# Optimization experiments

Hardware: AMD Instinct MI355X
Metric: run time of the kernel (lower is better)

Reference implementation:

```python
import jax, jax.numpy as jnp
import numpy as np

B, TQ, TK = 32, 2000, 512
BLANK_LOGPROB = -1.0
NEG = -1e9  # stand-in for -inf, safe under logsumexp grads


def setup_inputs() -> dict:
    key = jax.random.key(0)
    k1, k2, k3 = jax.random.split(key, 3)
    attn_logprob = jax.random.normal(k1, (B, TQ, TK), dtype=jnp.float32)
    in_lens = jax.random.randint(k2, (B,), 1, TK + 1, dtype=jnp.int32)
    # query (mel) lengths >= key (text) lengths so the CTC alignment exists
    out_lens = jax.random.randint(k3, (B,), TK, TQ + 1, dtype=jnp.int32)
    return {"attn_logprob": attn_logprob, "in_lens": in_lens, "out_lens": out_lens}


def _forward_sum_loss(attn_logprob, in_lens, out_lens):
    # attn_logprob: [B, Tq, Tk]
    Bb, Tq, Tk = attn_logprob.shape
    kl = jnp.clip(in_lens, 1, Tk).astype(jnp.int32)      # target lengths
    ql = jnp.clip(out_lens, 1, Tq).astype(jnp.int32)     # input lengths

    # pad a blank column at key index 0 (blank logit = blank_logprob)
    padded = jnp.pad(attn_logprob, ((0, 0), (0, 0), (1, 0)),
                     constant_values=BLANK_LOGPROB)       # [B, Tq, Tk+1]
    # per-sample log_softmax over the first kl+1 key entries (masked softmax)
    key_mask = jnp.arange(Tk + 1)[None, :] <= kl[:, None]  # [B, Tk+1]
    logp = jax.nn.log_softmax(jnp.where(key_mask[:, None, :], padded, NEG), axis=-1)

    # CTC with targets = [1..kl] (all distinct), blank = 0.
    # Extended state sequence: blank,1,blank,2,...,blank,kl,blank -> 2*kl+1 states.
    S = 2 * Tk + 1
    s = jnp.arange(S)
    label_idx = jnp.where(s % 2 == 1, (s + 1) // 2, 0)          # emission index per state
    state_valid = s[None, :] < (2 * kl[:, None] + 1)            # [B, S]
    skip_ok = (s % 2 == 1) & (s >= 2)                           # distinct labels -> skip allowed

    e0 = logp[:, 0, label_idx]                                  # [B, S]
    alpha0 = jnp.full((Bb, S), NEG, dtype=logp.dtype)
    alpha0 = alpha0.at[:, 0].set(e0[:, 0]).at[:, 1].set(e0[:, 1])

    def step(alpha, xs):
        logp_t, t = xs                                          # logp_t: [B, Tk+1]
        e_t = logp_t[:, label_idx]                              # [B, S]
        p0 = alpha
        p1 = jnp.pad(alpha[:, :-1], ((0, 0), (1, 0)), constant_values=NEG)
        p2 = jnp.pad(alpha[:, :-2], ((0, 0), (2, 0)), constant_values=NEG)
        p2 = jnp.where(skip_ok[None, :], p2, NEG)
        new = jax.nn.logsumexp(jnp.stack([p0, p1, p2]), axis=0) + e_t
        new = jnp.where(state_valid, new, NEG)
        alpha = jnp.where((t < ql)[:, None], new, alpha)        # freeze past each ql
        return alpha, None

    xs = (jnp.moveaxis(logp[:, 1:, :], 0, 1), jnp.arange(1, Tq))
    alpha, _ = jax.lax.scan(step, alpha0, xs)

    end = 2 * kl                                                # final blank state
    a_end = jnp.take_along_axis(alpha, end[:, None], axis=1)[:, 0]
    a_lab = jnp.take_along_axis(alpha, (end - 1)[:, None], axis=1)[:, 0]
    ll = jnp.logaddexp(a_end, a_lab)
    # torch CTCLoss(reduction='mean') with batch 1 divides by target length
    loss = -ll / kl.astype(attn_logprob.dtype)
    return jnp.mean(loss)


def reference(attn_logprob, in_lens, out_lens):
    return _forward_sum_loss(attn_logprob, in_lens, out_lens)
```

## Files before the change

### kernel.cpp

```cpp
#include <hip/hip_runtime.h>
#include <math.h>

#define BB 32
#define TQQ 2000
#define TKK 512
#define CR 8
#define RS 8
#define NW 8
#define SLOT_F 520
#define BRN 32

__device__ __forceinline__ float dpp_mv_111(float x, float old) {
    return __int_as_float(__builtin_amdgcn_update_dpp(__float_as_int(old), __float_as_int(x), 0x111, 0xf, 0xf, false));
}
__device__ __forceinline__ float dpp_mv_112(float x, float old) {
    return __int_as_float(__builtin_amdgcn_update_dpp(__float_as_int(old), __float_as_int(x), 0x112, 0xf, 0xf, false));
}
__device__ __forceinline__ float dpp_mv_114(float x, float old) {
    return __int_as_float(__builtin_amdgcn_update_dpp(__float_as_int(old), __float_as_int(x), 0x114, 0xf, 0xf, false));
}
__device__ __forceinline__ float dpp_mv_118(float x, float old) {
    return __int_as_float(__builtin_amdgcn_update_dpp(__float_as_int(old), __float_as_int(x), 0x118, 0xf, 0xf, false));
}
__device__ __forceinline__ float dpp_mv_b15(float x, float old) {
    return __int_as_float(__builtin_amdgcn_update_dpp(__float_as_int(old), __float_as_int(x), 0x142, 0xf, 0xf, false));
}
__device__ __forceinline__ float dpp_mv_b31(float x, float old) {
    return __int_as_float(__builtin_amdgcn_update_dpp(__float_as_int(old), __float_as_int(x), 0x143, 0xf, 0xf, false));
}
__device__ __forceinline__ float dpp_wave_shr1(float x, float old) {
    return __int_as_float(__builtin_amdgcn_update_dpp(__float_as_int(old), __float_as_int(x), 0x138, 0xf, 0xf, false));
}

__device__ __forceinline__ float wred_max(float x) {
    x = fmaxf(x, dpp_mv_111(x, -1e38f));
    x = fmaxf(x, dpp_mv_112(x, -1e38f));
    x = fmaxf(x, dpp_mv_114(x, -1e38f));
    x = fmaxf(x, dpp_mv_118(x, -1e38f));
    x = fmaxf(x, dpp_mv_b15(x, -1e38f));
    x = fmaxf(x, dpp_mv_b31(x, -1e38f));
    return __int_as_float(__builtin_amdgcn_readlane(__float_as_int(x), 63));
}
__device__ __forceinline__ float wred_sum(float x) {
    x += dpp_mv_111(x, 0.0f);
    x += dpp_mv_112(x, 0.0f);
    x += dpp_mv_114(x, 0.0f);
    x += dpp_mv_118(x, 0.0f);
    x += dpp_mv_b15(x, 0.0f);
    x += dpp_mv_b31(x, 0.0f);
    return __int_as_float(__builtin_amdgcn_readlane(__float_as_int(x), 63));
}

__device__ __forceinline__ float pow2i(int e) {
    return __int_as_float((unsigned)(e + 127) << 23);
}

__device__ __forceinline__ void step_quad(float4 p, float pb, float o_prev,
                                          float E[4], float O[4]) {
    float t3 = E[3] + O[2];  O[3] = (O[3] + t3) * p.w;  E[3] = t3 * pb;
    float t2 = E[2] + O[1];  O[2] = (O[2] + t2) * p.z;  E[2] = t2 * pb;
    float t1 = E[1] + O[0];  O[1] = (O[1] + t1) * p.y;  E[1] = t1 * pb;
    float t0 = E[0] + o_prev; O[0] = (O[0] + t0) * p.x; E[0] = t0 * pb;
}

__global__ __launch_bounds__(NW * 64)
void ForwardSumLoss_77378130805413_kernel(const float* __restrict__ attn,
                                          const int* __restrict__ in_lens,
                                          const int* __restrict__ out_lens,
                                          float* __restrict__ out)
{
    __shared__ float s_slots[RS * CR * SLOT_F];
    __shared__ float s_dumpE[513];
    __shared__ float s_dumpO[512];
    __shared__ float s_bring[BRN];
    __shared__ int   s_ef0[4];
    __shared__ int   s_ready[RS];
    __shared__ int   s_w0, s_w1;
    __shared__ int   s_e0c, s_e1c;

    const int b    = blockIdx.x;
    const int tid  = threadIdx.x;
    const int wave = tid >> 6;
    const int lane = tid & 63;

    int kl = in_lens[b];  kl = kl < 1 ? 1 : (kl > TKK ? TKK : kl);
    int ql = out_lens[b]; ql = ql < 1 ? 1 : (ql > TQQ ? TQQ : ql);
    const int nchunks = (ql + CR - 1) / CR;

    if (tid < RS)  s_ready[tid] = -1;
    if (tid < BRN) s_bring[tid] = 0.f;
    if (tid == 32) s_w0 = -1;
    if (tid == 33) s_w1 = -1;
    __syncthreads();

    volatile int* vready = s_ready;
    volatile int* vw0    = &s_w0;
    volatile int* vw1    = &s_w1;
    volatile int* vEF0   = s_ef0;

    const float T = 1.0995116e12f;

    if (wave == 0) {
        __builtin_amdgcn_s_setprio(3);
        float E[4] = {0,0,0,0}, O[4] = {0,0,0,0};
        int e0c = 0;
        const int base4 = 4 * lane;
        int rdyN = -9, w1s = -9;

        for (int k = 0; k < nchunks; ++k) {
            const int t0   = k * CR;
            const int rows = min(ql - t0, CR);
            if (k >= 2) { while (w1s < k - 2) { w1s = *vw1; } }
            if (rdyN != k) { while (vready[k & (RS - 1)] != k) {} }
            asm volatile("" ::: "memory");
            const float* bp = s_slots + (size_t)(k & (RS - 1)) * CR * SLOT_F;

            if (rows == CR) {
                float4 P[CR]; float PB[CR];
                #pragma unroll
                for (int r = 0; r < CR; ++r) {
                    P[r]  = *(const float4*)(bp + r * SLOT_F + base4);
                    PB[r] = bp[r * SLOT_F + 512];
                }
                rdyN = vready[(k + 1) & (RS - 1)];
                w1s  = *vw1;
                #pragma unroll
                for (int r = 0; r < CR; ++r) {
                    if (k == 0 && r == 0) {
                        E[0] = (lane == 0) ? PB[0]  * T : 0.f;
                        O[0] = (lane == 0) ? P[0].x * T : 0.f;
                    } else {
                        float o_prev = dpp_wave_shr1(O[3], 0.0f);
                        step_quad(P[r], PB[r], o_prev, E, O);
                    }
                    if (r < CR - 1) { if (lane == 63) s_bring[(t0 + r) & (BRN - 1)] = O[3]; }
                }
                float m0 = fmaxf(fmaxf(fmaxf(E[0], E[1]), fmaxf(E[2], E[3])),
                                 fmaxf(fmaxf(O[0], O[1]), fmaxf(O[2], O[3])));
                m0 = wred_max(m0);
                int ef = 0;
                if (m0 > 0.f) ef = 167 - (int)((__float_as_uint(m0) >> 23) & 255);
                float fh = pow2i(ef - (ef >> 1));
                float fl = pow2i(ef >> 1);
                #pragma unroll
                for (int i = 0; i < 4; ++i) { E[i] = (E[i] * fh) * fl; O[i] = (O[i] * fh) * fl; }
                e0c += ef;
                if (lane == 0) vEF0[k & 3] = ef;
                if (lane == 63) s_bring[(t0 + CR - 1) & (BRN - 1)] = O[3];
            } else {
                for (int r = 0; r < rows; ++r) {
                    const float* sq = bp + r * SLOT_F;
                    float4 p = *(const float4*)(sq + base4);
                    float pb = sq[512];
                    if (k == 0 && r == 0) {
                        E[0] = (lane == 0) ? pb  * T : 0.f;
                        O[0] = (lane == 0) ? p.x * T : 0.f;
                    } else {
                        float o_prev = dpp_wave_shr1(O[3], 0.0f);
                        step_quad(p, pb, o_prev, E, O);
                    }
                    if (lane == 63) s_bring[(t0 + r) & (BRN - 1)] = O[3];
                }
            }
            asm volatile("" ::: "memory");
            if (lane == 0) *vw0 = k;
        }
        #pragma unroll
        for (int i = 0; i < 4; ++i) {
            s_dumpE[base4 + i] = E[i];
            s_dumpO[base4 + i] = O[i];
        }
        if (lane == 0) s_e0c = e0c;
    } else if (wave == 1) {
        __builtin_amdgcn_s_setprio(3);
        float E[4] = {0,0,0,0}, O[4] = {0,0,0,0}, e512 = 0.f;
        int e0c = 0, e1c = 0;
        const int base4 = 256 + 4 * lane;
        int w0s = -9;

        for (int k = 0; k < nchunks; ++k) {
            const int t0   = k * CR;
            const int rows = min(ql - t0, CR);
            while (w0s < k) { w0s = *vw0; }
            asm volatile("" ::: "memory");
            const float* bp = s_slots + (size_t)(k & (RS - 1)) * CR * SLOT_F;

            int dE = e1c - e0c;
            dE = dE < -250 ? -250 : (dE > 250 ? 250 : dE);
            const float Ch = pow2i(dE - (dE >> 1));
            const float Cl = pow2i(dE >> 1);

            if (rows == CR) {
                float4 P[CR]; float PB[CR], BND[CR];
                #pragma unroll
                for (int r = 0; r < CR; ++r) {
                    P[r]   = *(const float4*)(bp + r * SLOT_F + base4);
                    PB[r]  = bp[r * SLOT_F + 512];
                    BND[r] = (s_bring[(t0 - 1 + r) & (BRN - 1)] * Ch) * Cl;
                }
                w0s = *vw0;
                #pragma unroll
                for (int r = 0; r < CR; ++r) {
                    float o_prev = dpp_wave_shr1(O[3], 0.0f);
                    o_prev = (lane == 0) ? BND[r] : o_prev;
                    float te = e512 + O[3]; e512 = te * PB[r];
                    step_quad(P[r], PB[r], o_prev, E, O);
                }
                float m1 = fmaxf(fmaxf(fmaxf(E[0], E[1]), fmaxf(E[2], E[3])),
                                 fmaxf(fmaxf(O[0], O[1]), fmaxf(O[2], O[3])));
                m1 = fmaxf(m1, e512);
                m1 = wred_max(m1);
                int ef0k = vEF0[k & 3];
                int ef1  = (m1 > 0.f) ? (167 - (int)((__float_as_uint(m1) >> 23) & 255))
                                      : ef0k;
                float fh = pow2i(ef1 - (ef1 >> 1));
                float fl = pow2i(ef1 >> 1);
                #pragma unroll
                for (int i = 0; i < 4; ++i) { E[i] = (E[i] * fh) * fl; O[i] = (O[i] * fh) * fl; }
                e512 = (e512 * fh) * fl;
                e1c += ef1;
                e0c += ef0k;
            } else {
                for (int r = 0; r < rows; ++r) {
                    const float* sq = bp + r * SLOT_F;
                    float4 p = *(const float4*)(sq + base4);
                    float pb = sq[512];
                    float bnd = (s_bring[(t0 - 1 + r) & (BRN - 1)] * Ch) * Cl;
                    float o_prev = dpp_wave_shr1(O[3], 0.0f);
                    o_prev = (lane == 0) ? bnd : o_prev;
                    float te = e512 + O[3]; e512 = te * pb;
                    step_quad(p, pb, o_prev, E, O);
                }
            }
            asm volatile("" ::: "memory");
            if (lane == 0) *vw1 = k;
        }
        #pragma unroll
        for (int i = 0; i < 4; ++i) {
            s_dumpE[base4 + i] = E[i];
            s_dumpO[base4 + i] = O[i];
        }
        if (lane == 63) s_dumpE[512] = e512;
        if (lane == 0)  s_e1c = e1c;
    } else {
        const int pidx = wave - 2;
        const float* base = attn + (size_t)b * TQQ * TKK;
        const int j0 = 8 * lane;

        for (int c = pidx; c < nchunks; c += NW - 2) {
            const int t0 = c * CR;
            while (*vw1 < c - RS) { __builtin_amdgcn_s_sleep(4); }
            asm volatile("" ::: "memory");

            float4 x0[CR], x1[CR];
            #pragma unroll
            for (int r = 0; r < CR; ++r) {
                x0[r] = make_float4(-1e30f, -1e30f, -1e30f, -1e30f);
                x1[r] = x0[r];
                const int t = t0 + r;
                if (t < ql) {
                    const float* row = base + (size_t)t * TKK;
                    if (j0 < kl)     x0[r] = *(const float4*)(row + j0);
                    if (j0 + 4 < kl) x1[r] = *(const float4*)(row + j0 + 4);
                }
            }
            float* bp = s_slots + (size_t)(c & (RS - 1)) * CR * SLOT_F;
            #pragma unroll
            for (int r = 0; r < CR; ++r) {
                const int t = t0 + r;
                if (t >= ql) continue;
                float va[8] = {x0[r].x, x0[r].y, x0[r].z, x0[r].w,
                               x1[r].x, x1[r].y, x1[r].z, x1[r].w};
                float m = -1.0f;
                #pragma unroll
                for (int cc = 0; cc < 8; ++cc) if (j0 + cc < kl) m = fmaxf(m, va[cc]);
                m = wred_max(m);
                float pv[8]; float vsum = 0.f;
                #pragma unroll
                for (int cc = 0; cc < 8; ++cc) {
                    pv[cc] = (j0 + cc < kl) ? __expf(va[cc] - m) : 0.f;
                    vsum += pv[cc];
                }
                vsum = wred_sum(vsum);
                float vb   = __expf(-1.0f - m);
                float rinv = 1.0f / (vsum + vb);
                float* sp = bp + (size_t)r * SLOT_F;
                *(float4*)(sp + j0)     = make_float4(pv[0]*rinv, pv[1]*rinv, pv[2]*rinv, pv[3]*rinv);
                *(float4*)(sp + j0 + 4) = make_float4(pv[4]*rinv, pv[5]*rinv, pv[6]*rinv, pv[7]*rinv);
                if (lane == 0) sp[512] = vb * rinv;
            }
            __threadfence_block();
            if (lane == 0) vready[c & (RS - 1)] = c;
        }
    }

    __syncthreads();
    if (tid == 0) {
        const double logTd = 27.725887222397812;
        const double LN2d  = 0.69314718055994531;
        float aE = s_dumpE[kl];
        float aO = s_dumpO[kl - 1];
        int e0c = s_e0c, e1c = s_e1c;
        double sE = logTd + (double)((kl     >= 256) ? e1c : e0c) * LN2d;
        double sO = logTd + (double)((kl - 1 >= 256) ? e1c : e0c) * LN2d;
        double lE = (aE > 0.f) ? log((double)aE) - sE : -1e300;
        double lO = (aO > 0.f) ? log((double)aO) - sO : -1e300;
        double mx = fmax(lE, lO);
        double ll = (mx < -1e290) ? -745.0 : mx + log(exp(lE - mx) + exp(lO - mx));
        float val = (float)(-ll / ((double)kl * (double)BB));
        atomicAdd(out, val);
    }
}

extern "C" void kernel_launch(void* const* d_in, const int* in_sizes, int n_in,
                              void* d_out, int out_size, void* d_ws, size_t ws_size,
                              hipStream_t stream) {
    const float* attn     = (const float*)d_in[0];
    const int*   in_lens  = (const int*)d_in[1];
    const int*   out_lens = (const int*)d_in[2];
    float* out = (float*)d_out;
    hipMemsetAsync(out, 0, sizeof(float), stream);
    hipLaunchKernelGGL(ForwardSumLoss_77378130805413_kernel,
                       dim3(BB), dim3(NW * 64), 0, stream,
                       attn, in_lens, out_lens, out);
}
```

Measured before the change: 370.5 us.

## Double-buffer LDS reads in recurrence waves with inline asm prefetch of next chunk

Both recurrence waves now prefetch the next chunk's probabilities, blank probs, boundary values and exponent offsets into a second register set with inline ds_read_b128, then wait on lgkmcnt before computing. This hides LDS latency behind the serial DP step. Blank probabilities and boundary carries move to contiguous per-slot arrays so each can be fetched as two vector reads. The producer/consumer lead between waves is relaxed from 2 to LEAD=5 chunks. In exchange, register pressure rises and correctness now depends on hand-managed waitcnt and sched_barrier ordering.

```diff
diff --git a/kernel.cpp b/kernel.cpp
--- a/kernel.cpp
+++ b/kernel.cpp
@@ -8,7 +8,11 @@
 #define RS 8
 #define NW 8
 #define SLOT_F 520
-#define BRN 32
+#define LEAD 5
+
+typedef float f32x4 __attribute__((ext_vector_type(4)));
+
+#define AS3F(p) ((const __attribute__((address_space(3))) float*)(p))
 
 __device__ __forceinline__ float dpp_mv_111(float x, float old) {
     return __int_as_float(__builtin_amdgcn_update_dpp(__float_as_int(old), __float_as_int(x), 0x111, 0xf, 0xf, false));
@@ -55,7 +59,7 @@
     return __int_as_float((unsigned)(e + 127) << 23);
 }
 
-__device__ __forceinline__ void step_quad(float4 p, float pb, float o_prev,
+__device__ __forceinline__ void step_quad(f32x4 p, float pb, float o_prev,
                                           float E[4], float O[4]) {
     float t3 = E[3] + O[2];  O[3] = (O[3] + t3) * p.w;  E[3] = t3 * pb;
     float t2 = E[2] + O[1];  O[2] = (O[2] + t2) * p.z;  E[2] = t2 * pb;
@@ -70,10 +74,11 @@
                                           float* __restrict__ out)
 {
     __shared__ float s_slots[RS * CR * SLOT_F];
+    __shared__ float s_pb[RS * CR];
+    __shared__ float s_bringS[RS * CR];
     __shared__ float s_dumpE[513];
     __shared__ float s_dumpO[512];
-    __shared__ float s_bring[BRN];
-    __shared__ int   s_ef0[4];
+    __shared__ int   s_ef0[RS];
     __shared__ int   s_ready[RS];
     __shared__ int   s_w0, s_w1;
     __shared__ int   s_e0c, s_e1c;
@@ -85,12 +90,13 @@
 
     int kl = in_lens[b];  kl = kl < 1 ? 1 : (kl > TKK ? TKK : kl);
     int ql = out_lens[b]; ql = ql < 1 ? 1 : (ql > TQQ ? TQQ : ql);
+    const int fullc   = ql >> 3;
     const int nchunks = (ql + CR - 1) / CR;
 
     if (tid < RS)  s_ready[tid] = -1;
-    if (tid < BRN) s_bring[tid] = 0.f;
-    if (tid == 32) s_w0 = -1;
-    if (tid == 33) s_w1 = -1;
+    if (tid >= 64 && tid < 64 + RS * CR) s_bringS[tid - 64] = 0.f;
+    if (tid == 128) s_w0 = -1;
+    if (tid == 129) s_w1 = -1;
     __syncthreads();
 
     volatile int* vready = s_ready;
@@ -105,66 +111,113 @@
         float E[4] = {0,0,0,0}, O[4] = {0,0,0,0};
         int e0c = 0;
         const int base4 = 4 * lane;
-        int rdyN = -9, w1s = -9;
-
-        for (int k = 0; k < nchunks; ++k) {
-            const int t0   = k * CR;
-            const int rows = min(ql - t0, CR);
-            if (k >= 2) { while (w1s < k - 2) { w1s = *vw1; } }
-            if (rdyN != k) { while (vready[k & (RS - 1)] != k) {} }
-            asm volatile("" ::: "memory");
-            const float* bp = s_slots + (size_t)(k & (RS - 1)) * CR * SLOT_F;
-
-            if (rows == CR) {
-                float4 P[CR]; float PB[CR];
-                #pragma unroll
-                for (int r = 0; r < CR; ++r) {
-                    P[r]  = *(const float4*)(bp + r * SLOT_F + base4);
-                    PB[r] = bp[r * SLOT_F + 512];
+        const unsigned aSlot0 = (unsigned)(unsigned long long)AS3F(s_slots) + (unsigned)(base4 * 4);
+        const unsigned aPbB   = (unsigned)(unsigned long long)AS3F(s_pb);
+        int rdyN = -9, w1s = -1;
+        int k = 0;
+
+        f32x4 A0={0,0,0,0},A1={0,0,0,0},A2={0,0,0,0},A3={0,0,0,0},A4={0,0,0,0},A5={0,0,0,0},A6={0,0,0,0},A7={0,0,0,0},Ap0={0,0,0,0},Ap1={0,0,0,0};
+        f32x4 B0={0,0,0,0},B1={0,0,0,0},B2={0,0,0,0},B3={0,0,0,0},B4={0,0,0,0},B5={0,0,0,0},B6={0,0,0,0},B7={0,0,0,0},Bp0={0,0,0,0},Bp1={0,0,0,0};
+
+#define W0_ISSUE(S, kk) do {                                                  \
+    unsigned a_ = aSlot0 + (unsigned)((((kk) & (RS - 1)) * CR * SLOT_F) * 4); \
+    asm volatile("ds_read_b128 %0, %1 offset:0"     : "=v"(S##0) : "v"(a_));  \
+    asm volatile("ds_read_b128 %0, %1 offset:2080"  : "=v"(S##1) : "v"(a_));  \
+    asm volatile("ds_read_b128 %0, %1 offset:4160"  : "=v"(S##2) : "v"(a_));  \
+    asm volatile("ds_read_b128 %0, %1 offset:6240"  : "=v"(S##3) : "v"(a_));  \
+    asm volatile("ds_read_b128 %0, %1 offset:8320"  : "=v"(S##4) : "v"(a_));  \
+    asm volatile("ds_read_b128 %0, %1 offset:10400" : "=v"(S##5) : "v"(a_));  \
+    asm volatile("ds_read_b128 %0, %1 offset:12480" : "=v"(S##6) : "v"(a_));  \
+    asm volatile("ds_read_b128 %0, %1 offset:14560" : "=v"(S##7) : "v"(a_));  \
+    unsigned q_ = aPbB + (unsigned)((((kk) & (RS - 1)) * CR) * 4);            \
+    asm volatile("ds_read_b128 %0, %1 offset:0"  : "=v"(S##p0) : "v"(q_));    \
+    asm volatile("ds_read_b128 %0, %1 offset:16" : "=v"(S##p1) : "v"(q_));    \
+} while (0)
+
+#define W0_STEP(CUR, NXT)                                                     \
+    do {                                                                      \
+        asm volatile("s_waitcnt lgkmcnt(0)" ::: "memory");                    \
+        __builtin_amdgcn_sched_barrier(0);                                    \
+        if (k + 1 < fullc) {                                                  \
+            if (rdyN != k + 1) {                                              \
+                do { rdyN = vready[(k + 1) & (RS - 1)]; } while (rdyN != k + 1); \
+                asm volatile("" ::: "memory");                                \
+            }                                                                 \
+            W0_ISSUE(NXT, k + 1);                                             \
+            __builtin_amdgcn_sched_barrier(0);                                \
+        }                                                                     \
+        if (w1s < k - LEAD) {                                                 \
+            do { w1s = *vw1; } while (w1s < k - LEAD);                        \
+            asm volatile("" ::: "memory");                                    \
+        }                                                                     \
+        {                                                                     \
+            f32x4 PA_[CR] = {CUR##0, CUR##1, CUR##2, CUR##3,                  \
+                             CUR##4, CUR##5, CUR##6, CUR##7};                 \
+            float PB_[CR] = {CUR##p0.x, CUR##p0.y, CUR##p0.z, CUR##p0.w,      \
+                             CUR##p1.x, CUR##p1.y, CUR##p1.z, CUR##p1.w};     \
+            _Pragma("unroll")                                                 \
+            for (int r = 0; r < CR; ++r) {                                    \
+                if (k == 0 && r == 0) {                                       \
+                    E[0] = (lane == 0) ? PB_[0]   * T : 0.f;                  \
+                    O[0] = (lane == 0) ? PA_[0].x * T : 0.f;                  \
+                } else {                                                      \
+                    float o_prev = dpp_wave_shr1(O[3], 0.0f);                 \
+                    step_quad(PA_[r], PB_[r], o_prev, E, O);                  \
+                }                                                             \
+                if (r < CR - 1) { if (lane == 63) s_bringS[(k & (RS - 1)) * CR + r] = O[3]; } \
+            }                                                                 \
+            float m0_ = fmaxf(fmaxf(fmaxf(E[0], E[1]), fmaxf(E[2], E[3])),    \
+                              fmaxf(fmaxf(O[0], O[1]), fmaxf(O[2], O[3])));   \
+            m0_ = wred_max(m0_);                                              \
+            int ef_ = 0;                                                      \
+            if (m0_ > 0.f) ef_ = 167 - (int)((__float_as_uint(m0_) >> 23) & 255); \
+            float fh_ = pow2i(ef_ - (ef_ >> 1));                              \
+            float fl_ = pow2i(ef_ >> 1);                                      \
+            _Pragma("unroll")                                                 \
+            for (int i = 0; i < 4; ++i) { E[i] = (E[i]*fh_)*fl_; O[i] = (O[i]*fh_)*fl_; } \
+            e0c += ef_;                                                       \
+            if (lane == 0) vEF0[k & (RS - 1)] = ef_;                          \
+            if (lane == 63) s_bringS[(k & (RS - 1)) * CR + (CR - 1)] = O[3];  \
+        }                                                                     \
+        asm volatile("" ::: "memory");                                        \
+        if (lane == 0) *vw0 = k;                                              \
+        w1s  = *vw1;                                                          \
+        rdyN = vready[(k + 2) & (RS - 1)];                                    \
+    } while (0)
+
+        if (fullc > 0) {
+            while (vready[0] != 0) {}
+            asm volatile("" ::: "memory");
+            W0_ISSUE(A, 0);
+            for (;;) {
+                W0_STEP(A, B); if (++k >= fullc) break;
+                W0_STEP(B, A); if (++k >= fullc) break;
+            }
+        }
+        if (nchunks > fullc) {
+            const int rows = ql - k * CR;
+            if (w1s < k - LEAD) { do { w1s = *vw1; } while (w1s < k - LEAD); }
+            while (vready[k & (RS - 1)] != k) {}
+            asm volatile("" ::: "memory");
+            const float* bp  = s_slots + (size_t)(k & (RS - 1)) * CR * SLOT_F;
+            const float* pbb = s_pb + (k & (RS - 1)) * CR;
+            for (int r = 0; r < rows; ++r) {
+                f32x4 pl = *(const f32x4*)(bp + r * SLOT_F + base4);
+                float pb = pbb[r];
+                if (k == 0 && r == 0) {
+                    E[0] = (lane == 0) ? pb   * T : 0.f;
+                    O[0] = (lane == 0) ? pl.x * T : 0.f;
+                } else {
+                    float o_prev = dpp_wave_shr1(O[3], 0.0f);
+                    step_quad(pl, pb, o_prev, E, O);
                 }
-                rdyN = vready[(k + 1) & (RS - 1)];
-                w1s  = *vw1;
-                #pragma unroll
-                for (int r = 0; r < CR; ++r) {
-                    if (k == 0 && r == 0) {
-                        E[0] = (lane == 0) ? PB[0]  * T : 0.f;
-                        O[0] = (lane == 0) ? P[0].x * T : 0.f;
-                    } else {
-                        float o_prev = dpp_wave_shr1(O[3], 0.0f);
-                        step_quad(P[r], PB[r], o_prev, E, O);
-                    }
-                    if (r < CR - 1) { if (lane == 63) s_bring[(t0 + r) & (BRN - 1)] = O[3]; }
-                }
-                float m0 = fmaxf(fmaxf(fmaxf(E[0], E[1]), fmaxf(E[2], E[3])),
-                                 fmaxf(fmaxf(O[0], O[1]), fmaxf(O[2], O[3])));
-                m0 = wred_max(m0);
-                int ef = 0;
-                if (m0 > 0.f) ef = 167 - (int)((__float_as_uint(m0) >> 23) & 255);
-                float fh = pow2i(ef - (ef >> 1));
-                float fl = pow2i(ef >> 1);
-                #pragma unroll
-                for (int i = 0; i < 4; ++i) { E[i] = (E[i] * fh) * fl; O[i] = (O[i] * fh) * fl; }
-                e0c += ef;
-                if (lane == 0) vEF0[k & 3] = ef;
-                if (lane == 63) s_bring[(t0 + CR - 1) & (BRN - 1)] = O[3];
-            } else {
-                for (int r = 0; r < rows; ++r) {
-                    const float* sq = bp + r * SLOT_F;
-                    float4 p = *(const float4*)(sq + base4);
-                    float pb = sq[512];
-                    if (k == 0 && r == 0) {
-                        E[0] = (lane == 0) ? pb  * T : 0.f;
-                        O[0] = (lane == 0) ? p.x * T : 0.f;
-                    } else {
-                        float o_prev = dpp_wave_shr1(O[3], 0.0f);
-                        step_quad(p, pb, o_prev, E, O);
-                    }
-                    if (lane == 63) s_bring[(t0 + r) & (BRN - 1)] = O[3];
-                }
+                if (lane == 63) s_bringS[(k & (RS - 1)) * CR + r] = O[3];
             }
             asm volatile("" ::: "memory");
             if (lane == 0) *vw0 = k;
         }
+#undef W0_STEP
+#undef W0_ISSUE
         #pragma unroll
         for (int i = 0; i < 4; ++i) {
             s_dumpE[base4 + i] = E[i];
@@ -173,68 +226,126 @@
         if (lane == 0) s_e0c = e0c;
     } else if (wave == 1) {
         __builtin_amdgcn_s_setprio(3);
-        float E[4] = {0,0,0,0}, O[4] = {0,0,0,0}, e512 = 0.f;
+        float E[4] = {0,0,0,0}, O[4] = {0,0,0,0}, e512 = 0.f, prev7 = 0.f;
         int e0c = 0, e1c = 0;
         const int base4 = 256 + 4 * lane;
-        int w0s = -9;
-
-        for (int k = 0; k < nchunks; ++k) {
-            const int t0   = k * CR;
-            const int rows = min(ql - t0, CR);
+        const unsigned aSlot0 = (unsigned)(unsigned long long)AS3F(s_slots) + (unsigned)(base4 * 4);
+        const unsigned aPbB   = (unsigned)(unsigned long long)AS3F(s_pb);
+        const unsigned aBrB   = (unsigned)(unsigned long long)AS3F(s_bringS);
+        const unsigned aEfB   = (unsigned)(unsigned long long)AS3F((const float*)s_ef0);
+        int w0s = -1;
+        int k = 0;
+
+        f32x4 A0={0,0,0,0},A1={0,0,0,0},A2={0,0,0,0},A3={0,0,0,0},A4={0,0,0,0},A5={0,0,0,0},A6={0,0,0,0},A7={0,0,0,0},Ap0={0,0,0,0},Ap1={0,0,0,0},Ab0={0,0,0,0},Ab1={0,0,0,0};
+        f32x4 B0={0,0,0,0},B1={0,0,0,0},B2={0,0,0,0},B3={0,0,0,0},B4={0,0,0,0},B5={0,0,0,0},B6={0,0,0,0},B7={0,0,0,0},Bp0={0,0,0,0},Bp1={0,0,0,0},Bb0={0,0,0,0},Bb1={0,0,0,0};
+        int Ae_ = 0, Be_ = 0;
+
+#define W1_ISSUE(S, kk) do {                                                  \
+    unsigned a_ = aSlot0 + (unsigned)((((kk) & (RS - 1)) * CR * SLOT_F) * 4); \
+    asm volatile("ds_read_b128 %0, %1 offset:0"     : "=v"(S##0) : "v"(a_));  \
+    asm volatile("ds_read_b128 %0, %1 offset:2080"  : "=v"(S##1) : "v"(a_));  \
+    asm volatile("ds_read_b128 %0, %1 offset:4160"  : "=v"(S##2) : "v"(a_));  \
+    asm volatile("ds_read_b128 %0, %1 offset:6240"  : "=v"(S##3) : "v"(a_));  \
+    asm volatile("ds_read_b128 %0, %1 offset:8320"  : "=v"(S##4) : "v"(a_));  \
+    asm volatile("ds_read_b128 %0, %1 offset:10400" : "=v"(S##5) : "v"(a_));  \
+    asm volatile("ds_read_b128 %0, %1 offset:12480" : "=v"(S##6) : "v"(a_));  \
+    asm volatile("ds_read_b128 %0, %1 offset:14560" : "=v"(S##7) : "v"(a_));  \
+    unsigned q_ = aPbB + (unsigned)((((kk) & (RS - 1)) * CR) * 4);            \
+    asm volatile("ds_read_b128 %0, %1 offset:0"  : "=v"(S##p0) : "v"(q_));    \
+    asm volatile("ds_read_b128 %0, %1 offset:16" : "=v"(S##p1) : "v"(q_));    \
+    unsigned r_ = aBrB + (unsigned)((((kk) & (RS - 1)) * CR) * 4);            \
+    asm volatile("ds_read_b128 %0, %1 offset:0"  : "=v"(S##b0) : "v"(r_));    \
+    asm volatile("ds_read_b128 %0, %1 offset:16" : "=v"(S##b1) : "v"(r_));    \
+    unsigned e_ = aEfB + (unsigned)(((kk) & (RS - 1)) * 4);                   \
+    asm volatile("ds_read_b32 %0, %1" : "=v"(S##e_) : "v"(e_));               \
+} while (0)
+
+#define W1_STEP(CUR, NXT)                                                     \
+    do {                                                                      \
+        asm volatile("s_waitcnt lgkmcnt(0)" ::: "memory");                    \
+        __builtin_amdgcn_sched_barrier(0);                                    \
+        if (k + 1 < fullc) {                                                  \
+            if (w0s < k + 1) {                                                \
+                do { w0s = *vw0; } while (w0s < k + 1);                       \
+                asm volatile("" ::: "memory");                                \
+            }                                                                 \
+            W1_ISSUE(NXT, k + 1);                                             \
+            __builtin_amdgcn_sched_barrier(0);                                \
+        }                                                                     \
+        {                                                                     \
+            int dE_ = e1c - e0c;                                              \
+            dE_ = dE_ < -250 ? -250 : (dE_ > 250 ? 250 : dE_);                \
+            const float Ch_ = pow2i(dE_ - (dE_ >> 1));                        \
+            const float Cl_ = pow2i(dE_ >> 1);                                \
+            int ef0k_ = CUR##e_;                                              \
+            f32x4 PA_[CR] = {CUR##0, CUR##1, CUR##2, CUR##3,                  \
+                             CUR##4, CUR##5, CUR##6, CUR##7};                 \
+            float PB_[CR] = {CUR##p0.x, CUR##p0.y, CUR##p0.z, CUR##p0.w,      \
+                             CUR##p1.x, CUR##p1.y, CUR##p1.z, CUR##p1.w};     \
+            float BR_[CR] = {prev7, CUR##b0.x, CUR##b0.y, CUR##b0.z,          \
+                             CUR##b0.w, CUR##b1.x, CUR##b1.y, CUR##b1.z};     \
+            _Pragma("unroll")                                                 \
+            for (int r = 0; r < CR; ++r) {                                    \
+                float bnd_ = (BR_[r] * Ch_) * Cl_;                            \
+                float o_prev = dpp_wave_shr1(O[3], 0.0f);                     \
+                o_prev = (lane == 0) ? bnd_ : o_prev;                         \
+                float te_ = e512 + O[3]; e512 = te_ * PB_[r];                 \
+                step_quad(PA_[r], PB_[r], o_prev, E, O);                      \
+            }                                                                 \
+            float m1_ = fmaxf(fmaxf(fmaxf(E[0], E[1]), fmaxf(E[2], E[3])),    \
+                              fmaxf(fmaxf(O[0], O[1]), fmaxf(O[2], O[3])));   \
+            m1_ = fmaxf(m1_, e512);                                           \
+            m1_ = wred_max(m1_);                                              \
+            int ef1_ = (m1_ > 0.f) ? (167 - (int)((__float_as_uint(m1_) >> 23) & 255)) \
+                                   : ef0k_;                                   \
+            float fh_ = pow2i(ef1_ - (ef1_ >> 1));                            \
+            float fl_ = pow2i(ef1_ >> 1);                                     \
+            _Pragma("unroll")                                                 \
+            for (int i = 0; i < 4; ++i) { E[i] = (E[i]*fh_)*fl_; O[i] = (O[i]*fh_)*fl_; } \
+            e512 = (e512 * fh_) * fl_;                                        \
+            e1c += ef1_;                                                      \
+            e0c += ef0k_;                                                     \
+            prev7 = CUR##b1.w;                                                \
+        }                                                                     \
+        asm volatile("" ::: "memory");                                        \
+        if (lane == 0) *vw1 = k;                                              \
+        w0s = *vw0;                                                           \
+    } while (0)
+
+        if (fullc > 0) {
+            do { w0s = *vw0; } while (w0s < 0);
+            asm volatile("" ::: "memory");
+            W1_ISSUE(A, 0);
+            for (;;) {
+                W1_STEP(A, B); if (++k >= fullc) break;
+                W1_STEP(B, A); if (++k >= fullc) break;
+            }
+        }
+        if (nchunks > fullc) {
+            const int rows = ql - k * CR;
             while (w0s < k) { w0s = *vw0; }
             asm volatile("" ::: "memory");
-            const float* bp = s_slots + (size_t)(k & (RS - 1)) * CR * SLOT_F;
-
             int dE = e1c - e0c;
             dE = dE < -250 ? -250 : (dE > 250 ? 250 : dE);
             const float Ch = pow2i(dE - (dE >> 1));
             const float Cl = pow2i(dE >> 1);
-
-            if (rows == CR) {
-                float4 P[CR]; float PB[CR], BND[CR];
-                #pragma unroll
-                for (int r = 0; r < CR; ++r) {
-                    P[r]   = *(const float4*)(bp + r * SLOT_F + base4);
-                    PB[r]  = bp[r * SLOT_F + 512];
-                    BND[r] = (s_bring[(t0 - 1 + r) & (BRN - 1)] * Ch) * Cl;
-                }
-                w0s = *vw0;
-                #pragma unroll
-                for (int r = 0; r < CR; ++r) {
-                    float o_prev = dpp_wave_shr1(O[3], 0.0f);
-                    o_prev = (lane == 0) ? BND[r] : o_prev;
-                    float te = e512 + O[3]; e512 = te * PB[r];
-                    step_quad(P[r], PB[r], o_prev, E, O);
-                }
-                float m1 = fmaxf(fmaxf(fmaxf(E[0], E[1]), fmaxf(E[2], E[3])),
-                                 fmaxf(fmaxf(O[0], O[1]), fmaxf(O[2], O[3])));
-                m1 = fmaxf(m1, e512);
-                m1 = wred_max(m1);
-                int ef0k = vEF0[k & 3];
-                int ef1  = (m1 > 0.f) ? (167 - (int)((__float_as_uint(m1) >> 23) & 255))
-                                      : ef0k;
-                float fh = pow2i(ef1 - (ef1 >> 1));
-                float fl = pow2i(ef1 >> 1);
-                #pragma unroll
-                for (int i = 0; i < 4; ++i) { E[i] = (E[i] * fh) * fl; O[i] = (O[i] * fh) * fl; }
-                e512 = (e512 * fh) * fl;
-                e1c += ef1;
-                e0c += ef0k;
-            } else {
-                for (int r = 0; r < rows; ++r) {
-                    const float* sq = bp + r * SLOT_F;
-                    float4 p = *(const float4*)(sq + base4);
-                    float pb = sq[512];
-                    float bnd = (s_bring[(t0 - 1 + r) & (BRN - 1)] * Ch) * Cl;
-                    float o_prev = dpp_wave_shr1(O[3], 0.0f);
-                    o_prev = (lane == 0) ? bnd : o_prev;
-                    float te = e512 + O[3]; e512 = te * pb;
-                    step_quad(p, pb, o_prev, E, O);
-                }
+            const float* bp  = s_slots + (size_t)(k & (RS - 1)) * CR * SLOT_F;
+            const float* pbb = s_pb + (k & (RS - 1)) * CR;
+            for (int r = 0; r < rows; ++r) {
+                f32x4 pl = *(const f32x4*)(bp + r * SLOT_F + base4);
+                float pb = pbb[r];
+                float braw = (r == 0) ? prev7 : s_bringS[(k & (RS - 1)) * CR + (r - 1)];
+                float bnd = (braw * Ch) * Cl;
+                float o_prev = dpp_wave_shr1(O[3], 0.0f);
+                o_prev = (lane == 0) ? bnd : o_prev;
+                float te = e512 + O[3]; e512 = te * pb;
+                step_quad(pl, pb, o_prev, E, O);
             }
             asm volatile("" ::: "memory");
             if (lane == 0) *vw1 = k;
         }
+#undef W1_STEP
+#undef W1_ISSUE
         #pragma unroll
         for (int i = 0; i < 4; ++i) {
             s_dumpE[base4 + i] = E[i];
@@ -287,7 +398,7 @@
                 float* sp = bp + (size_t)r * SLOT_F;
                 *(float4*)(sp + j0)     = make_float4(pv[0]*rinv, pv[1]*rinv, pv[2]*rinv, pv[3]*rinv);
                 *(float4*)(sp + j0 + 4) = make_float4(pv[4]*rinv, pv[5]*rinv, pv[6]*rinv, pv[7]*rinv);
-                if (lane == 0) sp[512] = vb * rinv;
+                if (lane == 0) s_pb[(c & (RS - 1)) * CR + r] = vb * rinv;
             }
             __threadfence_block();
             if (lane == 0) vready[c & (RS - 1)] = c;
```

Measured after the change: 411.0 us. +10.9%, slower.
